# Kernel tuning notes

Measured on AMD Instinct MI355X. Metric: run time of the kernel, lower is better.

## Reference

```python
import jax, jax.numpy as jnp
import numpy as np

N = 100000   # nodes
D = 128      # embedding_dim
E = 1600000  # edges
L = 3        # num_layers


def setup_inputs() -> dict:
    key = jax.random.key(0)
    ks = jax.random.split(key, 10)
    s = 1.0 / np.sqrt(D)
    def w(k, shape):
        return jax.random.uniform(k, shape, jnp.float32, -s, s)
    return {
        "x": jax.random.normal(ks[0], (N, D), jnp.float32),
        "edge_index": jax.random.randint(ks[1], (2, E), 0, N, jnp.int32),
        "Wp": w(ks[2], (L - 1, D, D)),   # project Linear weight (per layer)
        "bp": w(ks[3], (L - 1, D)),      # project Linear bias
        "Wl": w(ks[4], (L - 1, D, D)),   # lin_l (aggregated neighbors)
        "bl": w(ks[5], (L - 1, D)),
        "Wr": w(ks[6], (L - 1, D, D)),   # lin_r (root, no bias)
        "Wl_out": w(ks[7], (D, D)),
        "bl_out": w(ks[8], (D,)),
        "Wr_out": w(ks[9], (D, D)),
    }


def _sage(x, src, dst, inv_deg, Wl, bl, Wr, Wp=None, bp=None, normalize=False):
    # PyG SAGEConv: project applies to messages only; root term uses original x.
    h = jax.nn.relu(x @ Wp.T + bp) if Wp is not None else x
    agg = jax.ops.segment_sum(h[src], dst, num_segments=N) * inv_deg  # mean aggr
    out = agg @ Wl.T + bl + x @ Wr.T
    if normalize:
        out = out / jnp.maximum(
            jnp.linalg.norm(out, axis=-1, keepdims=True), 1e-12)
    return out


def reference(x, edge_index, Wp, bp, Wl, bl, Wr, Wl_out, bl_out, Wr_out):
    src, dst = edge_index[0], edge_index[1]
    deg = jax.ops.segment_sum(jnp.ones((src.shape[0],), x.dtype), dst,
                              num_segments=N)
    inv_deg = (1.0 / jnp.maximum(deg, 1.0))[:, None]  # isolated nodes -> 0 agg
    for i in range(L - 1):
        x = jax.nn.relu(
            _sage(x, src, dst, inv_deg, Wl[i], bl[i], Wr[i], Wp[i], bp[i],
                  normalize=True))
    return _sage(x, src, dst, inv_deg, Wl_out, bl_out, Wr_out)
```

## Files before the change

kernel.cpp:

```cpp
#include <hip/hip_runtime.h>
#include <math.h>

#define D 128

typedef short s8v __attribute__((ext_vector_type(8)));
typedef float f32x4 __attribute__((ext_vector_type(4)));
typedef unsigned short u16x8 __attribute__((ext_vector_type(8)));

__device__ __forceinline__ unsigned short f2bf(float f) {
  union { float f; unsigned u; } c; c.f = f;
  unsigned u = c.u;
  unsigned r = (u + 0x7fffu + ((u >> 16) & 1u)) >> 16;
  return (unsigned short)r;
}

__device__ __forceinline__ void gload_lds16(const void* g, void* l) {
  __builtin_amdgcn_global_load_lds((const __attribute__((address_space(1))) void*)g,
                                   (__attribute__((address_space(3))) void*)l, 16, 0, 0);
}

__global__ __launch_bounds__(256) void k_prep(const float* __restrict__ Wp,
                                              const float* __restrict__ Wl,
                                              const float* __restrict__ Wr,
                                              const float* __restrict__ Wlo,
                                              const float* __restrict__ Wro,
                                              unsigned short* __restrict__ Wb,
                                              const int* __restrict__ dst,
                                              int* __restrict__ bucketCnt, int E_) {
  int t = threadIdx.x;
  if (blockIdx.x < 128) {
    int i = blockIdx.x * 256 + t;
    const float* s;
    int off;
    if (i < 8192)       { s = Wp;  off = 0; }
    else if (i < 16384) { s = Wl;  off = 8192; }
    else if (i < 24576) { s = Wr;  off = 16384; }
    else if (i < 28672) { s = Wlo; off = 24576; }
    else                { s = Wro; off = 28672; }
    float4 a = ((const float4*)s)[i - off];
    ushort4 o;
    o.x = f2bf(a.x); o.y = f2bf(a.y); o.z = f2bf(a.z); o.w = f2bf(a.w);
    ((ushort4*)Wb)[i] = o;
  } else {
    __shared__ int hist[512];
    hist[t] = 0; hist[t + 256] = 0;
    __syncthreads();
    int base = (blockIdx.x - 128) * 4096;
#pragma unroll
    for (int i = 0; i < 16; i++) {
      int e = base + i * 256 + t;
      if (e < E_) atomicAdd(&hist[dst[e] >> 8], 1);
    }
    __syncthreads();
    int c = hist[t];       if (c) atomicAdd(&bucketCnt[t], c);
    c = hist[t + 256];     if (c) atomicAdd(&bucketCnt[t + 256], c);
  }
}

__global__ __launch_bounds__(512) void k_bucket_scan(const int* __restrict__ cnt,
                                                     int* __restrict__ base,
                                                     int* __restrict__ cursor,
                                                     int* __restrict__ row_start,
                                                     int n, int E_) {
  __shared__ int bs[512];
  int t = threadIdx.x;
  int orig = cnt[t];
  bs[t] = orig;
  __syncthreads();
  for (int off = 1; off < 512; off <<= 1) {
    int x = (t >= off) ? bs[t - off] : 0;
    __syncthreads();
    bs[t] += x;
    __syncthreads();
  }
  int ex = bs[t] - orig;
  base[t] = ex;
  cursor[t] = ex;
  if (t == 511) base[512] = bs[511];
  if (t == 0) row_start[n] = E_;
}

__global__ __launch_bounds__(1024) void k_partA(const int* __restrict__ src,
                                                const int* __restrict__ dst,
                                                int* __restrict__ cursor,
                                                unsigned* __restrict__ pairs, int E_) {
  __shared__ int hist[512];
  __shared__ int gbase[512];
  int t = threadIdx.x;
  int base = blockIdx.x * 16384;
  if (t < 512) hist[t] = 0;
  __syncthreads();
  unsigned p_[16];
  int k_[16];
#pragma unroll
  for (int i = 0; i < 16; i++) {
    int e = base + i * 1024 + t;
    if (e < E_) {
      int s = src[e], d = dst[e];
      p_[i] = ((unsigned)s << 8) | (unsigned)(d & 255);
      k_[i] = d >> 8;
      atomicAdd(&hist[k_[i]], 1);
    } else {
      k_[i] = -1;
    }
  }
  __syncthreads();
  if (t < 512) {
    int c = hist[t];
    gbase[t] = c ? atomicAdd(&cursor[t], c) : 0;
    hist[t] = 0;
  }
  __syncthreads();
#pragma unroll
  for (int i = 0; i < 16; i++) {
    if (k_[i] >= 0) {
      int r = atomicAdd(&hist[k_[i]], 1);
      pairs[gbase[k_[i]] + r] = p_[i];
    }
  }
}

__device__ __forceinline__ int swz_chunk(int r, int c) { return (r << 4) + (c ^ (r & 7)); }

__global__ __launch_bounds__(1024, 4) void k_proj0B(const float* __restrict__ Av,
                                                    const unsigned short* __restrict__ W,
                                                    const float* __restrict__ bias,
                                                    unsigned short* __restrict__ out,
                                                    unsigned short* __restrict__ xb_out,
                                                    const unsigned* __restrict__ pairs,
                                                    const int* __restrict__ bucketBase,
                                                    int* __restrict__ row_start,
                                                    int* __restrict__ csr,
                                                    int n, int nP) {
  __shared__ __align__(16) unsigned short Wlds[128 * 128];
  __shared__ int cnt[256];
  __shared__ int scn[256];
  int t = threadIdx.x;

  if ((int)blockIdx.x < nP) {
    int wv = t >> 6, l = t & 63, lg = l >> 4, ln = l & 15;
    int rb = blockIdx.x * 256 + wv * 16;
    int arow = rb + ln;
    if (arow >= n) arow = n - 1;

    s8v a[4];
    const float* Af = Av + (size_t)arow * D + lg * 8;
#pragma unroll
    for (int ks = 0; ks < 4; ++ks) {
      float4 f0 = *(const float4*)(Af + ks * 32);
      float4 f1 = *(const float4*)(Af + ks * 32 + 4);
      s8v av;
      av[0] = (short)f2bf(f0.x); av[1] = (short)f2bf(f0.y);
      av[2] = (short)f2bf(f0.z); av[3] = (short)f2bf(f0.w);
      av[4] = (short)f2bf(f1.x); av[5] = (short)f2bf(f1.y);
      av[6] = (short)f2bf(f1.z); av[7] = (short)f2bf(f1.w);
      a[ks] = av;
      *(s8v*)(xb_out + (size_t)arow * D + lg * 8 + ks * 32) = av;
    }

#pragma unroll
    for (int i = 0; i < 2; ++i) {
      int idx = t + i * 1024;
      int r = idx >> 4, k = idx & 15;
      int c = k ^ (r & 7);
      gload_lds16(W + r * 128 + c * 8, &Wlds[idx * 8]);
    }
    __syncthreads();

    f32x4 acc[8];
#pragma unroll
    for (int f = 0; f < 8; ++f) acc[f] = (f32x4){0.f, 0.f, 0.f, 0.f};
#pragma unroll
    for (int ks = 0; ks < 4; ++ks) {
#pragma unroll
      for (int f = 0; f < 8; ++f) {
        s8v b = *(const s8v*)&Wlds[swz_chunk(f * 16 + ln, ks * 4 + lg) * 8];
        acc[f] = __builtin_amdgcn_mfma_f32_16x16x32_bf16(a[ks], b, acc[f], 0, 0, 0);
      }
    }

#pragma unroll
    for (int r = 0; r < 4; ++r) {
      int gr = rb + 4 * lg + r;
      if (gr < n) {
#pragma unroll
        for (int f = 0; f < 8; ++f) {
          int c = f * 16 + ln;
          float v = acc[f][r] + bias[c];
          v = fmaxf(v, 0.f);
          out[(size_t)gr * D + c] = f2bf(v);
        }
      }
    }
  } else {
    int k = blockIdx.x - nP;
    int node0 = k << 8;
    int pbeg = bucketBase[k], pend = bucketBase[k + 1];
    if (t < 256) cnt[t] = 0;
    __syncthreads();
    for (int p = pbeg + t; p < pend; p += 1024) atomicAdd(&cnt[pairs[p] & 255], 1);
    __syncthreads();
    int c = 0;
    if (t < 256) { c = cnt[t]; scn[t] = c; }
    __syncthreads();
    for (int off = 1; off < 256; off <<= 1) {
      int xv = 0;
      if (t < 256 && t >= off) xv = scn[t - off];
      __syncthreads();
      if (t < 256) scn[t] += xv;
      __syncthreads();
    }
    if (t < 256) {
      int ex = scn[t] - c;
      int node = node0 + t;
      if (node < n) row_start[node] = pbeg + ex;
      cnt[t] = pbeg + ex;
    }
    __syncthreads();
    for (int p = pbeg + t; p < pend; p += 1024) {
      unsigned pr = pairs[p];
      int slot = atomicAdd(&cnt[pr & 255], 1);
      csr[slot] = (int)(pr >> 8);
    }
  }
}

__global__ __launch_bounds__(256) void k_aggregate(const unsigned short* __restrict__ h,
                                                   unsigned short* __restrict__ agg,
                                                   const int* __restrict__ row_start,
                                                   const int* __restrict__ csr, int n) {
  int node = (blockIdx.x * 256 + threadIdx.x) >> 4;
  int li = threadIdx.x & 15;
  if (node >= n) return;
  int rs0 = row_start[node];
  int dc = row_start[node + 1] - rs0;
  const int* ce = csr + rs0;
  const char* base = (const char*)h + li * 16;

  float accL[4], accH[4];
#pragma unroll
  for (int q = 0; q < 4; q++) { accL[q] = 0.f; accH[q] = 0.f; }

#define ACCR(v)                                                        \
  {                                                                    \
    unsigned dw[4] = {(v).x, (v).y, (v).z, (v).w};                     \
    _Pragma("unroll") for (int q = 0; q < 4; q++) {                    \
      accL[q] += __uint_as_float(dw[q] << 16);                         \
      accH[q] += __uint_as_float(dw[q] & 0xffff0000u);                 \
    }                                                                  \
  }

  int e = 0;
  bool more = (3 < dc);
  int s0 = 0, s1 = 0, s2 = 0, s3 = 0;
  if (more) { s0 = ce[0]; s1 = ce[1]; s2 = ce[2]; s3 = ce[3]; }
  while (more) {
    uint4 v0 = *(const uint4*)(base + (size_t)s0 * 256);
    uint4 v1 = *(const uint4*)(base + (size_t)s1 * 256);
    uint4 v2 = *(const uint4*)(base + (size_t)s2 * 256);
    uint4 v3 = *(const uint4*)(base + (size_t)s3 * 256);
    e += 4;
    more = (e + 3 < dc);
    if (more) { s0 = ce[e]; s1 = ce[e + 1]; s2 = ce[e + 2]; s3 = ce[e + 3]; }
    ACCR(v0); ACCR(v1); ACCR(v2); ACCR(v3);
  }
  if (e < dc)     { uint4 v = *(const uint4*)(base + (size_t)ce[e] * 256);     ACCR(v); }
  if (e + 1 < dc) { uint4 v = *(const uint4*)(base + (size_t)ce[e + 1] * 256); ACCR(v); }
  if (e + 2 < dc) { uint4 v = *(const uint4*)(base + (size_t)ce[e + 2] * 256); ACCR(v); }
#undef ACCR

  float iv = 1.0f / (float)(dc > 0 ? dc : 1);
  u16x8 o;
#pragma unroll
  for (int q = 0; q < 4; q++) {
    o[2 * q] = f2bf(accL[q] * iv);
    o[2 * q + 1] = f2bf(accH[q] * iv);
  }
  *(u16x8*)(agg + (size_t)node * D + li * 8) = o;
}

__global__ __launch_bounds__(512, 4) void k_gemm_proj(const unsigned short* __restrict__ A,
                                                      const unsigned short* __restrict__ W,
                                                      const float* __restrict__ bias,
                                                      unsigned short* __restrict__ out,
                                                      int n) {
  __shared__ __align__(16) unsigned short Wlds[128 * 128];
  int t = threadIdx.x;
  int wv = t >> 6, l = t & 63, lg = l >> 4, ln = l & 15;
  int rb = blockIdx.x * 128 + wv * 16;
  int arow = rb + ln;
  if (arow >= n) arow = n - 1;

  const s8v* Ap = (const s8v*)(A + (size_t)arow * D + lg * 8);
  s8v a[4];
#pragma unroll
  for (int ks = 0; ks < 4; ++ks) a[ks] = Ap[ks * 4];

#pragma unroll
  for (int i = 0; i < 4; ++i) {
    int idx = t + i * 512;
    int r = idx >> 4, k = idx & 15;
    int c = k ^ (r & 7);
    gload_lds16(W + r * 128 + c * 8, &Wlds[idx * 8]);
  }
  __syncthreads();

  f32x4 acc[8];
#pragma unroll
  for (int f = 0; f < 8; ++f) acc[f] = (f32x4){0.f, 0.f, 0.f, 0.f};
#pragma unroll
  for (int ks = 0; ks < 4; ++ks) {
#pragma unroll
    for (int f = 0; f < 8; ++f) {
      s8v b = *(const s8v*)&Wlds[swz_chunk(f * 16 + ln, ks * 4 + lg) * 8];
      acc[f] = __builtin_amdgcn_mfma_f32_16x16x32_bf16(a[ks], b, acc[f], 0, 0, 0);
    }
  }

#pragma unroll
  for (int r = 0; r < 4; ++r) {
    int gr = rb + 4 * lg + r;
    if (gr < n) {
#pragma unroll
      for (int f = 0; f < 8; ++f) {
        int c = f * 16 + ln;
        float v = acc[f][r] + bias[c];
        v = fmaxf(v, 0.f);
        out[(size_t)gr * D + c] = f2bf(v);
      }
    }
  }
}

template <int MODE>
__global__ __launch_bounds__(512, 4) void k_gemm_dual(const unsigned short* __restrict__ A1,
                                                      const unsigned short* __restrict__ W1,
                                                      const float* __restrict__ bias,
                                                      const unsigned short* __restrict__ A2,
                                                      const unsigned short* __restrict__ W2,
                                                      void* __restrict__ outv, int n) {
  __shared__ __align__(16) unsigned short Wlds[2 * 128 * 128];
  int t = threadIdx.x;
  int wv = t >> 6, l = t & 63, lg = l >> 4, ln = l & 15;
  int rb = blockIdx.x * 128 + wv * 16;
  int arow = rb + ln;
  if (arow >= n) arow = n - 1;
  const s8v* A1p = (const s8v*)(A1 + (size_t)arow * D + lg * 8);
  const s8v* A2p = (const s8v*)(A2 + (size_t)arow * D + lg * 8);
  s8v a1[4], a2[4];
#pragma unroll
  for (int ks = 0; ks < 4; ++ks) { a1[ks] = A1p[ks * 4]; a2[ks] = A2p[ks * 4]; }

#pragma unroll
  for (int i = 0; i < 8; ++i) {
    int idx = t + i * 512;
    int mat = idx >> 11;
    int rem = idx & 2047;
    int r = rem >> 4, k = rem & 15;
    int c = k ^ (r & 7);
    const unsigned short* src = (mat ? W2 : W1) + r * 128 + c * 8;
    gload_lds16(src, &Wlds[idx * 8]);
  }
  __syncthreads();

  f32x4 acc[8];
#pragma unroll
  for (int f = 0; f < 8; ++f) acc[f] = (f32x4){0.f, 0.f, 0.f, 0.f};

#pragma unroll
  for (int ks = 0; ks < 4; ++ks) {
#pragma unroll
    for (int f = 0; f < 8; ++f) {
      int ch = swz_chunk(f * 16 + ln, ks * 4 + lg) * 8;
      s8v b1 = *(const s8v*)&Wlds[ch];
      s8v b2 = *(const s8v*)&Wlds[16384 + ch];
      acc[f] = __builtin_amdgcn_mfma_f32_16x16x32_bf16(a1[ks], b1, acc[f], 0, 0, 0);
      acc[f] = __builtin_amdgcn_mfma_f32_16x16x32_bf16(a2[ks], b2, acc[f], 0, 0, 0);
    }
  }

#pragma unroll
  for (int r = 0; r < 4; ++r) {
    int gr = rb + 4 * lg + r;
    float v[8];
#pragma unroll
    for (int f = 0; f < 8; ++f) v[f] = acc[f][r] + bias[f * 16 + ln];
    if (MODE == 0) {
      float ss = 0.f;
#pragma unroll
      for (int f = 0; f < 8; ++f) ss += v[f] * v[f];
      ss += __shfl_xor(ss, 1);
      ss += __shfl_xor(ss, 2);
      ss += __shfl_xor(ss, 4);
      ss += __shfl_xor(ss, 8);
      float sc = 1.0f / fmaxf(sqrtf(ss), 1e-12f);
      if (gr < n) {
        unsigned short* out = (unsigned short*)outv;
#pragma unroll
        for (int f = 0; f < 8; ++f) {
          float o = fmaxf(v[f] * sc, 0.f);
          out[(size_t)gr * D + f * 16 + ln] = f2bf(o);
        }
      }
    } else {
      if (gr < n) {
        float* out = (float*)outv;
#pragma unroll
        for (int f = 0; f < 8; ++f) out[(size_t)gr * D + f * 16 + ln] = v[f];
      }
    }
  }
}

extern "C" void kernel_launch(void* const* d_in, const int* in_sizes, int n_in,
                              void* d_out, int out_size, void* d_ws, size_t ws_size,
                              hipStream_t stream) {
  const float* x   = (const float*)d_in[0];
  const int*   ei  = (const int*)d_in[1];
  const float* Wp  = (const float*)d_in[2];
  const float* bp  = (const float*)d_in[3];
  const float* Wl  = (const float*)d_in[4];
  const float* bl  = (const float*)d_in[5];
  const float* Wr  = (const float*)d_in[6];
  const float* Wlo = (const float*)d_in[7];
  const float* blo = (const float*)d_in[8];
  const float* Wro = (const float*)d_in[9];

  const int N = in_sizes[0] / D;
  const int E = in_sizes[1] / 2;
  const int* srcIdx = ei;
  const int* dstIdx = ei + E;

  const size_t ND = (size_t)N * D;

  unsigned short* xb   = (unsigned short*)d_ws;
  unsigned short* h    = xb + ND;
  unsigned short* aggB = h + ND;
  unsigned short* x2   = aggB + ND;
  unsigned short* Wb   = x2 + ND;
  int* row_start  = (int*)(Wb + 8 * 16384);
  int* bucketCnt  = row_start + N + 1;
  int* bucketBase = bucketCnt + 512;
  int* cursor     = bucketBase + 513;
  int* csr        = cursor + 512;

  unsigned* pairs = (unsigned*)aggB;

  unsigned short* Wpb0 = Wb;
  unsigned short* Wpb1 = Wb + 16384;
  unsigned short* Wlb0 = Wb + 2 * 16384;
  unsigned short* Wlb1 = Wb + 3 * 16384;
  unsigned short* Wrb0 = Wb + 4 * 16384;
  unsigned short* Wrb1 = Wb + 5 * 16384;
  unsigned short* Wlob = Wb + 6 * 16384;
  unsigned short* Wrob = Wb + 7 * 16384;

  unsigned short* x1 = (unsigned short*)d_out;

  int gG  = (N + 127) / 128;
  int gP  = (N + 255) / 256;
  int gAg = (N * 16 + 255) / 256;
  int KB  = (N + 255) / 256;
  int gBC = (E + 4095) / 4096;
  int gA  = (E + 16383) / 16384;

  hipMemsetAsync(bucketCnt, 0, 512 * sizeof(int), stream);
  k_prep<<<128 + gBC, 256, 0, stream>>>(Wp, Wl, Wr, Wlo, Wro, Wb, dstIdx, bucketCnt, E);

  k_bucket_scan<<<1, 512, 0, stream>>>(bucketCnt, bucketBase, cursor, row_start, N, E);
  k_partA<<<gA, 1024, 0, stream>>>(srcIdx, dstIdx, cursor, pairs, E);

  k_proj0B<<<gP + KB, 1024, 0, stream>>>(x, Wpb0, bp, h, xb,
                                         pairs, bucketBase, row_start, csr, N, gP);

  k_aggregate<<<gAg, 256, 0, stream>>>(h, aggB, row_start, csr, N);
  k_gemm_dual<0><<<gG, 512, 0, stream>>>(aggB, Wlb0, bl, xb, Wrb0, (void*)x1, N);

  k_gemm_proj<<<gG, 512, 0, stream>>>(x1, Wpb1, bp + D, h, N);
  k_aggregate<<<gAg, 256, 0, stream>>>(h, aggB, row_start, csr, N);
  k_gemm_dual<0><<<gG, 512, 0, stream>>>(aggB, Wlb1, bl + D, x1, Wrb1, (void*)x2, N);

  k_aggregate<<<gAg, 256, 0, stream>>>(x2, aggB, row_start, csr, N);
  k_gemm_dual<1><<<gG, 512, 0, stream>>>(aggB, Wlob, blo, x2, Wrob, d_out, N);
}
```

Baseline: 323.6 us.

## Fuse neighbor aggregation with dual GEMM and regroup CSR build kernels

Aggregation is fused with the following lin_l/lin_r dual GEMM: each 256-thread block gathers 16 nodes' neighbor means into a swizzled LDS tile, then four waves each compute two 16-column output fragments, with L2 normalization reduced across waves through shared memory. This removes the bf16 agg buffer write and reread per layer and one launch per layer. Weights are now read straight from global memory per block instead of being staged in LDS, and each block does only a small GEMM, which adds redundant weight traffic. Separately, partition-A is co-scheduled with the layer-0 projection in one launch, and partition-B becomes its own kernel.

```diff
diff --git a/kernel.cpp b/kernel.cpp
--- a/kernel.cpp
+++ b/kernel.cpp
@@ -80,66 +80,60 @@
   if (t == 0) row_start[n] = E_;
 }
 
-__global__ __launch_bounds__(1024) void k_partA(const int* __restrict__ src,
-                                                const int* __restrict__ dst,
-                                                int* __restrict__ cursor,
-                                                unsigned* __restrict__ pairs, int E_) {
+__device__ __forceinline__ int swz_chunk(int r, int c) { return (r << 4) + (c ^ (r & 7)); }
+
+__global__ __launch_bounds__(1024, 2) void k_partA_proj(const int* __restrict__ src,
+                                                        const int* __restrict__ dst,
+                                                        int* __restrict__ cursor,
+                                                        unsigned* __restrict__ pairs,
+                                                        int E_,
+                                                        const float* __restrict__ Av,
+                                                        const unsigned short* __restrict__ W,
+                                                        const float* __restrict__ bias,
+                                                        unsigned short* __restrict__ out,
+                                                        unsigned short* __restrict__ xb_out,
+                                                        int n, int nA) {
   __shared__ int hist[512];
   __shared__ int gbase[512];
+  __shared__ __align__(16) unsigned short Wlds[128 * 128];
   int t = threadIdx.x;
-  int base = blockIdx.x * 16384;
-  if (t < 512) hist[t] = 0;
-  __syncthreads();
-  unsigned p_[16];
-  int k_[16];
-#pragma unroll
-  for (int i = 0; i < 16; i++) {
-    int e = base + i * 1024 + t;
-    if (e < E_) {
-      int s = src[e], d = dst[e];
-      p_[i] = ((unsigned)s << 8) | (unsigned)(d & 255);
-      k_[i] = d >> 8;
-      atomicAdd(&hist[k_[i]], 1);
-    } else {
-      k_[i] = -1;
-    }
-  }
-  __syncthreads();
-  if (t < 512) {
-    int c = hist[t];
-    gbase[t] = c ? atomicAdd(&cursor[t], c) : 0;
-    hist[t] = 0;
-  }
-  __syncthreads();
-#pragma unroll
-  for (int i = 0; i < 16; i++) {
-    if (k_[i] >= 0) {
-      int r = atomicAdd(&hist[k_[i]], 1);
-      pairs[gbase[k_[i]] + r] = p_[i];
-    }
-  }
-}
-
-__device__ __forceinline__ int swz_chunk(int r, int c) { return (r << 4) + (c ^ (r & 7)); }
-
-__global__ __launch_bounds__(1024, 4) void k_proj0B(const float* __restrict__ Av,
-                                                    const unsigned short* __restrict__ W,
-                                                    const float* __restrict__ bias,
-                                                    unsigned short* __restrict__ out,
-                                                    unsigned short* __restrict__ xb_out,
-                                                    const unsigned* __restrict__ pairs,
-                                                    const int* __restrict__ bucketBase,
-                                                    int* __restrict__ row_start,
-                                                    int* __restrict__ csr,
-                                                    int n, int nP) {
-  __shared__ __align__(16) unsigned short Wlds[128 * 128];
-  __shared__ int cnt[256];
-  __shared__ int scn[256];
-  int t = threadIdx.x;
-
-  if ((int)blockIdx.x < nP) {
+
+  if ((int)blockIdx.x < nA) {
+    int base = blockIdx.x * 16384;
+    if (t < 512) hist[t] = 0;
+    __syncthreads();
+    unsigned p_[16];
+    int k_[16];
+#pragma unroll
+    for (int i = 0; i < 16; i++) {
+      int e = base + i * 1024 + t;
+      if (e < E_) {
+        int s = src[e], d = dst[e];
+        p_[i] = ((unsigned)s << 8) | (unsigned)(d & 255);
+        k_[i] = d >> 8;
+        atomicAdd(&hist[k_[i]], 1);
+      } else {
+        k_[i] = -1;
+      }
+    }
+    __syncthreads();
+    if (t < 512) {
+      int c = hist[t];
+      gbase[t] = c ? atomicAdd(&cursor[t], c) : 0;
+      hist[t] = 0;
+    }
+    __syncthreads();
+#pragma unroll
+    for (int i = 0; i < 16; i++) {
+      if (k_[i] >= 0) {
+        int r = atomicAdd(&hist[k_[i]], 1);
+        pairs[gbase[k_[i]] + r] = p_[i];
+      }
+    }
+  } else {
+    int bid = blockIdx.x - nA;
     int wv = t >> 6, l = t & 63, lg = l >> 4, ln = l & 15;
-    int rb = blockIdx.x * 256 + wv * 16;
+    int rb = bid * 256 + wv * 16;
     int arow = rb + ln;
     if (arow >= n) arow = n - 1;
 
@@ -192,50 +186,68 @@
         }
       }
     }
-  } else {
-    int k = blockIdx.x - nP;
-    int node0 = k << 8;
-    int pbeg = bucketBase[k], pend = bucketBase[k + 1];
-    if (t < 256) cnt[t] = 0;
-    __syncthreads();
-    for (int p = pbeg + t; p < pend; p += 1024) atomicAdd(&cnt[pairs[p] & 255], 1);
-    __syncthreads();
-    int c = 0;
-    if (t < 256) { c = cnt[t]; scn[t] = c; }
-    __syncthreads();
-    for (int off = 1; off < 256; off <<= 1) {
-      int xv = 0;
-      if (t < 256 && t >= off) xv = scn[t - off];
-      __syncthreads();
-      if (t < 256) scn[t] += xv;
-      __syncthreads();
-    }
-    if (t < 256) {
-      int ex = scn[t] - c;
-      int node = node0 + t;
-      if (node < n) row_start[node] = pbeg + ex;
-      cnt[t] = pbeg + ex;
-    }
-    __syncthreads();
-    for (int p = pbeg + t; p < pend; p += 1024) {
-      unsigned pr = pairs[p];
-      int slot = atomicAdd(&cnt[pr & 255], 1);
-      csr[slot] = (int)(pr >> 8);
-    }
-  }
-}
-
-__global__ __launch_bounds__(256) void k_aggregate(const unsigned short* __restrict__ h,
-                                                   unsigned short* __restrict__ agg,
-                                                   const int* __restrict__ row_start,
-                                                   const int* __restrict__ csr, int n) {
-  int node = (blockIdx.x * 256 + threadIdx.x) >> 4;
-  int li = threadIdx.x & 15;
-  if (node >= n) return;
+  }
+}
+
+__global__ __launch_bounds__(1024) void k_partB(const unsigned* __restrict__ pairs,
+                                                const int* __restrict__ bucketBase,
+                                                int* __restrict__ row_start,
+                                                int* __restrict__ csr, int n) {
+  __shared__ int cnt[256];
+  __shared__ int scn[256];
+  int k = blockIdx.x, t = threadIdx.x;
+  int node0 = k << 8;
+  int pbeg = bucketBase[k], pend = bucketBase[k + 1];
+  if (t < 256) cnt[t] = 0;
+  __syncthreads();
+  for (int p = pbeg + t; p < pend; p += 1024) atomicAdd(&cnt[pairs[p] & 255], 1);
+  __syncthreads();
+  int c = 0;
+  if (t < 256) { c = cnt[t]; scn[t] = c; }
+  __syncthreads();
+  for (int off = 1; off < 256; off <<= 1) {
+    int xv = 0;
+    if (t < 256 && t >= off) xv = scn[t - off];
+    __syncthreads();
+    if (t < 256) scn[t] += xv;
+    __syncthreads();
+  }
+  if (t < 256) {
+    int ex = scn[t] - c;
+    int node = node0 + t;
+    if (node < n) row_start[node] = pbeg + ex;
+    cnt[t] = pbeg + ex;
+  }
+  __syncthreads();
+  for (int p = pbeg + t; p < pend; p += 1024) {
+    unsigned pr = pairs[p];
+    int slot = atomicAdd(&cnt[pr & 255], 1);
+    csr[slot] = (int)(pr >> 8);
+  }
+}
+
+template <int MODE>
+__global__ __launch_bounds__(256) void k_agg_dual(const unsigned short* __restrict__ h,
+                                                  const int* __restrict__ row_start,
+                                                  const int* __restrict__ csr,
+                                                  const unsigned short* __restrict__ W1,
+                                                  const float* __restrict__ bias,
+                                                  const unsigned short* __restrict__ A2,
+                                                  const unsigned short* __restrict__ W2,
+                                                  void* __restrict__ outv, int n) {
+  __shared__ __align__(16) unsigned short tile[16 * 128];
+  __shared__ float ssP[4][16];
+  int t = threadIdx.x;
+  int nodeLoc = t >> 4;
+  int li = t & 15;
+  int node0 = blockIdx.x * 16;
+  int node = node0 + nodeLoc;
+  if (node >= n) node = n - 1;
+
   int rs0 = row_start[node];
   int dc = row_start[node + 1] - rs0;
   const int* ce = csr + rs0;
-  const char* base = (const char*)h + li * 16;
+  const char* gbase = (const char*)h + li * 16;
 
   float accL[4], accH[4];
 #pragma unroll
@@ -255,28 +267,106 @@
   int s0 = 0, s1 = 0, s2 = 0, s3 = 0;
   if (more) { s0 = ce[0]; s1 = ce[1]; s2 = ce[2]; s3 = ce[3]; }
   while (more) {
-    uint4 v0 = *(const uint4*)(base + (size_t)s0 * 256);
-    uint4 v1 = *(const uint4*)(base + (size_t)s1 * 256);
-    uint4 v2 = *(const uint4*)(base + (size_t)s2 * 256);
-    uint4 v3 = *(const uint4*)(base + (size_t)s3 * 256);
+    uint4 v0 = *(const uint4*)(gbase + (size_t)s0 * 256);
+    uint4 v1 = *(const uint4*)(gbase + (size_t)s1 * 256);
+    uint4 v2 = *(const uint4*)(gbase + (size_t)s2 * 256);
+    uint4 v3 = *(const uint4*)(gbase + (size_t)s3 * 256);
     e += 4;
     more = (e + 3 < dc);
     if (more) { s0 = ce[e]; s1 = ce[e + 1]; s2 = ce[e + 2]; s3 = ce[e + 3]; }
     ACCR(v0); ACCR(v1); ACCR(v2); ACCR(v3);
   }
-  if (e < dc)     { uint4 v = *(const uint4*)(base + (size_t)ce[e] * 256);     ACCR(v); }
-  if (e + 1 < dc) { uint4 v = *(const uint4*)(base + (size_t)ce[e + 1] * 256); ACCR(v); }
-  if (e + 2 < dc) { uint4 v = *(const uint4*)(base + (size_t)ce[e + 2] * 256); ACCR(v); }
+  if (e < dc)     { uint4 v = *(const uint4*)(gbase + (size_t)ce[e] * 256);     ACCR(v); }
+  if (e + 1 < dc) { uint4 v = *(const uint4*)(gbase + (size_t)ce[e + 1] * 256); ACCR(v); }
+  if (e + 2 < dc) { uint4 v = *(const uint4*)(gbase + (size_t)ce[e + 2] * 256); ACCR(v); }
 #undef ACCR
 
   float iv = 1.0f / (float)(dc > 0 ? dc : 1);
-  u16x8 o;
-#pragma unroll
-  for (int q = 0; q < 4; q++) {
-    o[2 * q] = f2bf(accL[q] * iv);
-    o[2 * q + 1] = f2bf(accH[q] * iv);
-  }
-  *(u16x8*)(agg + (size_t)node * D + li * 8) = o;
+  {
+    u16x8 o;
+#pragma unroll
+    for (int q = 0; q < 4; q++) {
+      o[2 * q] = f2bf(accL[q] * iv);
+      o[2 * q + 1] = f2bf(accH[q] * iv);
+    }
+    *(u16x8*)&tile[swz_chunk(nodeLoc, li) * 8] = o;
+  }
+  __syncthreads();
+
+  int wv = t >> 6, l = t & 63, lg = l >> 4, ln = l & 15;
+  int a2row = node0 + ln;
+  if (a2row >= n) a2row = n - 1;
+  s8v a1[4], a2[4];
+#pragma unroll
+  for (int ks = 0; ks < 4; ++ks) {
+    a1[ks] = *(const s8v*)&tile[swz_chunk(ln, ks * 4 + lg) * 8];
+    a2[ks] = *(const s8v*)(A2 + (size_t)a2row * D + lg * 8 + ks * 32);
+  }
+
+  f32x4 acc[2];
+  acc[0] = (f32x4){0.f, 0.f, 0.f, 0.f};
+  acc[1] = (f32x4){0.f, 0.f, 0.f, 0.f};
+#pragma unroll
+  for (int ks = 0; ks < 4; ++ks) {
+#pragma unroll
+    for (int ff = 0; ff < 2; ++ff) {
+      int f = wv * 2 + ff;
+      s8v b1 = *(const s8v*)(W1 + (size_t)(f * 16 + ln) * D + lg * 8 + ks * 32);
+      s8v b2 = *(const s8v*)(W2 + (size_t)(f * 16 + ln) * D + lg * 8 + ks * 32);
+      acc[ff] = __builtin_amdgcn_mfma_f32_16x16x32_bf16(a1[ks], b1, acc[ff], 0, 0, 0);
+      acc[ff] = __builtin_amdgcn_mfma_f32_16x16x32_bf16(a2[ks], b2, acc[ff], 0, 0, 0);
+    }
+  }
+
+  float v[2][4];
+#pragma unroll
+  for (int ff = 0; ff < 2; ++ff)
+#pragma unroll
+    for (int r = 0; r < 4; ++r) v[ff][r] = acc[ff][r] + bias[(wv * 2 + ff) * 16 + ln];
+
+  if (MODE == 0) {
+    float ssr[4];
+#pragma unroll
+    for (int r = 0; r < 4; ++r) ssr[r] = v[0][r] * v[0][r] + v[1][r] * v[1][r];
+#pragma unroll
+    for (int r = 0; r < 4; ++r) {
+      ssr[r] += __shfl_xor(ssr[r], 1);
+      ssr[r] += __shfl_xor(ssr[r], 2);
+      ssr[r] += __shfl_xor(ssr[r], 4);
+      ssr[r] += __shfl_xor(ssr[r], 8);
+    }
+    if (ln == 0) {
+#pragma unroll
+      for (int r = 0; r < 4; ++r) ssP[wv][lg * 4 + r] = ssr[r];
+    }
+    __syncthreads();
+    unsigned short* out = (unsigned short*)outv;
+#pragma unroll
+    for (int r = 0; r < 4; ++r) {
+      int row = lg * 4 + r;
+      int gr = node0 + row;
+      float ss = ssP[0][row] + ssP[1][row] + ssP[2][row] + ssP[3][row];
+      float sc = 1.0f / fmaxf(sqrtf(ss), 1e-12f);
+      if (gr < n) {
+#pragma unroll
+        for (int ff = 0; ff < 2; ++ff) {
+          float o = fmaxf(v[ff][r] * sc, 0.f);
+          out[(size_t)gr * D + (wv * 2 + ff) * 16 + ln] = f2bf(o);
+        }
+      }
+    }
+  } else {
+    float* out = (float*)outv;
+#pragma unroll
+    for (int r = 0; r < 4; ++r) {
+      int gr = node0 + lg * 4 + r;
+      if (gr < n) {
+#pragma unroll
+        for (int ff = 0; ff < 2; ++ff)
+          out[(size_t)gr * D + (wv * 2 + ff) * 16 + ln] = v[ff][r];
+      }
+    }
+  }
 }
 
 __global__ __launch_bounds__(512, 4) void k_gemm_proj(const unsigned short* __restrict__ A,
@@ -327,86 +417,6 @@
         float v = acc[f][r] + bias[c];
         v = fmaxf(v, 0.f);
         out[(size_t)gr * D + c] = f2bf(v);
-      }
-    }
-  }
-}
-
-template <int MODE>
-__global__ __launch_bounds__(512, 4) void k_gemm_dual(const unsigned short* __restrict__ A1,
-                                                      const unsigned short* __restrict__ W1,
-                                                      const float* __restrict__ bias,
-                                                      const unsigned short* __restrict__ A2,
-                                                      const unsigned short* __restrict__ W2,
-                                                      void* __restrict__ outv, int n) {
-  __shared__ __align__(16) unsigned short Wlds[2 * 128 * 128];
-  int t = threadIdx.x;
-  int wv = t >> 6, l = t & 63, lg = l >> 4, ln = l & 15;
-  int rb = blockIdx.x * 128 + wv * 16;
-  int arow = rb + ln;
-  if (arow >= n) arow = n - 1;
-  const s8v* A1p = (const s8v*)(A1 + (size_t)arow * D + lg * 8);
-  const s8v* A2p = (const s8v*)(A2 + (size_t)arow * D + lg * 8);
-  s8v a1[4], a2[4];
-#pragma unroll
-  for (int ks = 0; ks < 4; ++ks) { a1[ks] = A1p[ks * 4]; a2[ks] = A2p[ks * 4]; }
-
-#pragma unroll
-  for (int i = 0; i < 8; ++i) {
-    int idx = t + i * 512;
-    int mat = idx >> 11;
-    int rem = idx & 2047;
-    int r = rem >> 4, k = rem & 15;
-    int c = k ^ (r & 7);
-    const unsigned short* src = (mat ? W2 : W1) + r * 128 + c * 8;
-    gload_lds16(src, &Wlds[idx * 8]);
-  }
-  __syncthreads();
-
-  f32x4 acc[8];
-#pragma unroll
-  for (int f = 0; f < 8; ++f) acc[f] = (f32x4){0.f, 0.f, 0.f, 0.f};
-
-#pragma unroll
-  for (int ks = 0; ks < 4; ++ks) {
-#pragma unroll
-    for (int f = 0; f < 8; ++f) {
-      int ch = swz_chunk(f * 16 + ln, ks * 4 + lg) * 8;
-      s8v b1 = *(const s8v*)&Wlds[ch];
-      s8v b2 = *(const s8v*)&Wlds[16384 + ch];
-      acc[f] = __builtin_amdgcn_mfma_f32_16x16x32_bf16(a1[ks], b1, acc[f], 0, 0, 0);
-      acc[f] = __builtin_amdgcn_mfma_f32_16x16x32_bf16(a2[ks], b2, acc[f], 0, 0, 0);
-    }
-  }
-
-#pragma unroll
-  for (int r = 0; r < 4; ++r) {
-    int gr = rb + 4 * lg + r;
-    float v[8];
-#pragma unroll
-    for (int f = 0; f < 8; ++f) v[f] = acc[f][r] + bias[f * 16 + ln];
-    if (MODE == 0) {
-      float ss = 0.f;
-#pragma unroll
-      for (int f = 0; f < 8; ++f) ss += v[f] * v[f];
-      ss += __shfl_xor(ss, 1);
-      ss += __shfl_xor(ss, 2);
-      ss += __shfl_xor(ss, 4);
-      ss += __shfl_xor(ss, 8);
-      float sc = 1.0f / fmaxf(sqrtf(ss), 1e-12f);
-      if (gr < n) {
-        unsigned short* out = (unsigned short*)outv;
-#pragma unroll
-        for (int f = 0; f < 8; ++f) {
-          float o = fmaxf(v[f] * sc, 0.f);
-          out[(size_t)gr * D + f * 16 + ln] = f2bf(o);
-        }
-      }
-    } else {
-      if (gr < n) {
-        float* out = (float*)outv;
-#pragma unroll
-        for (int f = 0; f < 8; ++f) out[(size_t)gr * D + f * 16 + ln] = v[f];
       }
     }
   }
@@ -459,27 +469,26 @@
 
   int gG  = (N + 127) / 128;
   int gP  = (N + 255) / 256;
-  int gAg = (N * 16 + 255) / 256;
+  int gF  = (N + 15) / 16;
   int KB  = (N + 255) / 256;
   int gBC = (E + 4095) / 4096;
   int gA  = (E + 16383) / 16384;
 
   hipMemsetAsync(bucketCnt, 0, 512 * sizeof(int), stream);
   k_prep<<<128 + gBC, 256, 0, stream>>>(Wp, Wl, Wr, Wlo, Wro, Wb, dstIdx, bucketCnt, E);
-
   k_bucket_scan<<<1, 512, 0, stream>>>(bucketCnt, bucketBase, cursor, row_start, N, E);
-  k_partA<<<gA, 1024, 0, stream>>>(srcIdx, dstIdx, cursor, pairs, E);
-
-  k_proj0B<<<gP + KB, 1024, 0, stream>>>(x, Wpb0, bp, h, xb,
-                                         pairs, bucketBase, row_start, csr, N, gP);
-
-  k_aggregate<<<gAg, 256, 0, stream>>>(h, aggB, row_start, csr, N);
-  k_gemm_dual<0><<<gG, 512, 0, stream>>>(aggB, Wlb0, bl, xb, Wrb0, (void*)x1, N);
+
+  k_partA_proj<<<gA + gP, 1024, 0, stream>>>(srcIdx, dstIdx, cursor, pairs, E,
+                                             x, Wpb0, bp, h, xb, N, gA);
+  k_partB<<<KB, 1024, 0, stream>>>(pairs, bucketBase, row_start, csr, N);
+
+  k_agg_dual<0><<<gF, 256, 0, stream>>>(h, row_start, csr, Wlb0, bl, xb, Wrb0,
+                                        (void*)x1, N);
 
   k_gemm_proj<<<gG, 512, 0, stream>>>(x1, Wpb1, bp + D, h, N);
-  k_aggregate<<<gAg, 256, 0, stream>>>(h, aggB, row_start, csr, N);
-  k_gemm_dual<0><<<gG, 512, 0, stream>>>(aggB, Wlb1, bl + D, x1, Wrb1, (void*)x2, N);
-
-  k_aggregate<<<gAg, 256, 0, stream>>>(x2, aggB, row_start, csr, N);
-  k_gemm_dual<1><<<gG, 512, 0, stream>>>(aggB, Wlob, blo, x2, Wrob, d_out, N);
-}
+  k_agg_dual<0><<<gF, 256, 0, stream>>>(h, row_start, csr, Wlb1, bl + D, x1, Wrb1,
+                                        (void*)x2, N);
+
+  k_agg_dual<1><<<gF, 256, 0, stream>>>(x2, row_start, csr, Wlob, blo, x2, Wrob,
+                                        d_out, N);
+}
```

New measurement: 379.3 us. 1.17x slower.

## Regroup setup kernels and fuse layer-1 combine with layer-2 projection

Applied to the files above, without the earlier changes.

The edge partition pass (partA) now runs in the same launch as the first-layer input projection, and the CSR finalize pass (partB) becomes its own kernel. The layer-1 dual GEMM with normalize/ReLU is fused with the layer-2 projection GEMM, so the block rereads its own freshly written x1 rows instead of launching a separate kernel. This removes one launch and a round trip of x1 between kernels, at the cost of more LDS per block and a second serial GEMM phase inside the fused kernel. The fused kernel relies on a vmcnt wait plus a barrier so each block sees its own global writes of x1.

```diff
diff --git a/kernel.cpp b/kernel.cpp
--- a/kernel.cpp
+++ b/kernel.cpp
@@ -80,66 +80,60 @@
   if (t == 0) row_start[n] = E_;
 }
 
-__global__ __launch_bounds__(1024) void k_partA(const int* __restrict__ src,
-                                                const int* __restrict__ dst,
-                                                int* __restrict__ cursor,
-                                                unsigned* __restrict__ pairs, int E_) {
+__device__ __forceinline__ int swz_chunk(int r, int c) { return (r << 4) + (c ^ (r & 7)); }
+
+__global__ __launch_bounds__(1024, 2) void k_partA_proj(const int* __restrict__ src,
+                                                        const int* __restrict__ dst,
+                                                        int* __restrict__ cursor,
+                                                        unsigned* __restrict__ pairs,
+                                                        int E_,
+                                                        const float* __restrict__ Av,
+                                                        const unsigned short* __restrict__ W,
+                                                        const float* __restrict__ bias,
+                                                        unsigned short* __restrict__ out,
+                                                        unsigned short* __restrict__ xb_out,
+                                                        int n, int nA) {
   __shared__ int hist[512];
   __shared__ int gbase[512];
+  __shared__ __align__(16) unsigned short Wlds[128 * 128];
   int t = threadIdx.x;
-  int base = blockIdx.x * 16384;
-  if (t < 512) hist[t] = 0;
-  __syncthreads();
-  unsigned p_[16];
-  int k_[16];
-#pragma unroll
-  for (int i = 0; i < 16; i++) {
-    int e = base + i * 1024 + t;
-    if (e < E_) {
-      int s = src[e], d = dst[e];
-      p_[i] = ((unsigned)s << 8) | (unsigned)(d & 255);
-      k_[i] = d >> 8;
-      atomicAdd(&hist[k_[i]], 1);
-    } else {
-      k_[i] = -1;
-    }
-  }
-  __syncthreads();
-  if (t < 512) {
-    int c = hist[t];
-    gbase[t] = c ? atomicAdd(&cursor[t], c) : 0;
-    hist[t] = 0;
-  }
-  __syncthreads();
-#pragma unroll
-  for (int i = 0; i < 16; i++) {
-    if (k_[i] >= 0) {
-      int r = atomicAdd(&hist[k_[i]], 1);
-      pairs[gbase[k_[i]] + r] = p_[i];
-    }
-  }
-}
-
-__device__ __forceinline__ int swz_chunk(int r, int c) { return (r << 4) + (c ^ (r & 7)); }
-
-__global__ __launch_bounds__(1024, 4) void k_proj0B(const float* __restrict__ Av,
-                                                    const unsigned short* __restrict__ W,
-                                                    const float* __restrict__ bias,
-                                                    unsigned short* __restrict__ out,
-                                                    unsigned short* __restrict__ xb_out,
-                                                    const unsigned* __restrict__ pairs,
-                                                    const int* __restrict__ bucketBase,
-                                                    int* __restrict__ row_start,
-                                                    int* __restrict__ csr,
-                                                    int n, int nP) {
-  __shared__ __align__(16) unsigned short Wlds[128 * 128];
-  __shared__ int cnt[256];
-  __shared__ int scn[256];
-  int t = threadIdx.x;
-
-  if ((int)blockIdx.x < nP) {
+
+  if ((int)blockIdx.x < nA) {
+    int base = blockIdx.x * 16384;
+    if (t < 512) hist[t] = 0;
+    __syncthreads();
+    unsigned p_[16];
+    int k_[16];
+#pragma unroll
+    for (int i = 0; i < 16; i++) {
+      int e = base + i * 1024 + t;
+      if (e < E_) {
+        int s = src[e], d = dst[e];
+        p_[i] = ((unsigned)s << 8) | (unsigned)(d & 255);
+        k_[i] = d >> 8;
+        atomicAdd(&hist[k_[i]], 1);
+      } else {
+        k_[i] = -1;
+      }
+    }
+    __syncthreads();
+    if (t < 512) {
+      int c = hist[t];
+      gbase[t] = c ? atomicAdd(&cursor[t], c) : 0;
+      hist[t] = 0;
+    }
+    __syncthreads();
+#pragma unroll
+    for (int i = 0; i < 16; i++) {
+      if (k_[i] >= 0) {
+        int r = atomicAdd(&hist[k_[i]], 1);
+        pairs[gbase[k_[i]] + r] = p_[i];
+      }
+    }
+  } else {
+    int bid = blockIdx.x - nA;
     int wv = t >> 6, l = t & 63, lg = l >> 4, ln = l & 15;
-    int rb = blockIdx.x * 256 + wv * 16;
+    int rb = bid * 256 + wv * 16;
     int arow = rb + ln;
     if (arow >= n) arow = n - 1;
 
@@ -192,36 +186,43 @@
         }
       }
     }
-  } else {
-    int k = blockIdx.x - nP;
-    int node0 = k << 8;
-    int pbeg = bucketBase[k], pend = bucketBase[k + 1];
-    if (t < 256) cnt[t] = 0;
-    __syncthreads();
-    for (int p = pbeg + t; p < pend; p += 1024) atomicAdd(&cnt[pairs[p] & 255], 1);
-    __syncthreads();
-    int c = 0;
-    if (t < 256) { c = cnt[t]; scn[t] = c; }
-    __syncthreads();
-    for (int off = 1; off < 256; off <<= 1) {
-      int xv = 0;
-      if (t < 256 && t >= off) xv = scn[t - off];
-      __syncthreads();
-      if (t < 256) scn[t] += xv;
-      __syncthreads();
-    }
-    if (t < 256) {
-      int ex = scn[t] - c;
-      int node = node0 + t;
-      if (node < n) row_start[node] = pbeg + ex;
-      cnt[t] = pbeg + ex;
-    }
-    __syncthreads();
-    for (int p = pbeg + t; p < pend; p += 1024) {
-      unsigned pr = pairs[p];
-      int slot = atomicAdd(&cnt[pr & 255], 1);
-      csr[slot] = (int)(pr >> 8);
-    }
+  }
+}
+
+__global__ __launch_bounds__(1024) void k_partB(const unsigned* __restrict__ pairs,
+                                                const int* __restrict__ bucketBase,
+                                                int* __restrict__ row_start,
+                                                int* __restrict__ csr, int n) {
+  __shared__ int cnt[256];
+  __shared__ int scn[256];
+  int k = blockIdx.x, t = threadIdx.x;
+  int node0 = k << 8;
+  int pbeg = bucketBase[k], pend = bucketBase[k + 1];
+  if (t < 256) cnt[t] = 0;
+  __syncthreads();
+  for (int p = pbeg + t; p < pend; p += 1024) atomicAdd(&cnt[pairs[p] & 255], 1);
+  __syncthreads();
+  int c = 0;
+  if (t < 256) { c = cnt[t]; scn[t] = c; }
+  __syncthreads();
+  for (int off = 1; off < 256; off <<= 1) {
+    int xv = 0;
+    if (t < 256 && t >= off) xv = scn[t - off];
+    __syncthreads();
+    if (t < 256) scn[t] += xv;
+    __syncthreads();
+  }
+  if (t < 256) {
+    int ex = scn[t] - c;
+    int node = node0 + t;
+    if (node < n) row_start[node] = pbeg + ex;
+    cnt[t] = pbeg + ex;
+  }
+  __syncthreads();
+  for (int p = pbeg + t; p < pend; p += 1024) {
+    unsigned pr = pairs[p];
+    int slot = atomicAdd(&cnt[pr & 255], 1);
+    csr[slot] = (int)(pr >> 8);
   }
 }
 
@@ -277,59 +278,6 @@
     o[2 * q + 1] = f2bf(accH[q] * iv);
   }
   *(u16x8*)(agg + (size_t)node * D + li * 8) = o;
-}
-
-__global__ __launch_bounds__(512, 4) void k_gemm_proj(const unsigned short* __restrict__ A,
-                                                      const unsigned short* __restrict__ W,
-                                                      const float* __restrict__ bias,
-                                                      unsigned short* __restrict__ out,
-                                                      int n) {
-  __shared__ __align__(16) unsigned short Wlds[128 * 128];
-  int t = threadIdx.x;
-  int wv = t >> 6, l = t & 63, lg = l >> 4, ln = l & 15;
-  int rb = blockIdx.x * 128 + wv * 16;
-  int arow = rb + ln;
-  if (arow >= n) arow = n - 1;
-
-  const s8v* Ap = (const s8v*)(A + (size_t)arow * D + lg * 8);
-  s8v a[4];
-#pragma unroll
-  for (int ks = 0; ks < 4; ++ks) a[ks] = Ap[ks * 4];
-
-#pragma unroll
-  for (int i = 0; i < 4; ++i) {
-    int idx = t + i * 512;
-    int r = idx >> 4, k = idx & 15;
-    int c = k ^ (r & 7);
-    gload_lds16(W + r * 128 + c * 8, &Wlds[idx * 8]);
-  }
-  __syncthreads();
-
-  f32x4 acc[8];
-#pragma unroll
-  for (int f = 0; f < 8; ++f) acc[f] = (f32x4){0.f, 0.f, 0.f, 0.f};
-#pragma unroll
-  for (int ks = 0; ks < 4; ++ks) {
-#pragma unroll
-    for (int f = 0; f < 8; ++f) {
-      s8v b = *(const s8v*)&Wlds[swz_chunk(f * 16 + ln, ks * 4 + lg) * 8];
-      acc[f] = __builtin_amdgcn_mfma_f32_16x16x32_bf16(a[ks], b, acc[f], 0, 0, 0);
-    }
-  }
-
-#pragma unroll
-  for (int r = 0; r < 4; ++r) {
-    int gr = rb + 4 * lg + r;
-    if (gr < n) {
-#pragma unroll
-      for (int f = 0; f < 8; ++f) {
-        int c = f * 16 + ln;
-        float v = acc[f][r] + bias[c];
-        v = fmaxf(v, 0.f);
-        out[(size_t)gr * D + c] = f2bf(v);
-      }
-    }
-  }
 }
 
 template <int MODE>
@@ -412,6 +360,123 @@
   }
 }
 
+__global__ __launch_bounds__(512, 4) void k_dual_proj(const unsigned short* __restrict__ A1,
+                                                      const unsigned short* __restrict__ W1,
+                                                      const float* __restrict__ bias,
+                                                      const unsigned short* __restrict__ A2,
+                                                      const unsigned short* __restrict__ W2,
+                                                      unsigned short* __restrict__ x1out,
+                                                      const unsigned short* __restrict__ Wp,
+                                                      const float* __restrict__ biasP,
+                                                      unsigned short* __restrict__ hout,
+                                                      int n) {
+  __shared__ __align__(16) unsigned short Wlds[2 * 128 * 128];
+  int t = threadIdx.x;
+  int wv = t >> 6, l = t & 63, lg = l >> 4, ln = l & 15;
+  int rb = blockIdx.x * 128 + wv * 16;
+  int arow = rb + ln;
+  if (arow >= n) arow = n - 1;
+  const s8v* A1p = (const s8v*)(A1 + (size_t)arow * D + lg * 8);
+  const s8v* A2p = (const s8v*)(A2 + (size_t)arow * D + lg * 8);
+  s8v a1[4], a2[4];
+#pragma unroll
+  for (int ks = 0; ks < 4; ++ks) { a1[ks] = A1p[ks * 4]; a2[ks] = A2p[ks * 4]; }
+
+#pragma unroll
+  for (int i = 0; i < 8; ++i) {
+    int idx = t + i * 512;
+    int mat = idx >> 11;
+    int rem = idx & 2047;
+    int r = rem >> 4, k = rem & 15;
+    int c = k ^ (r & 7);
+    const unsigned short* src = (mat ? W2 : W1) + r * 128 + c * 8;
+    gload_lds16(src, &Wlds[idx * 8]);
+  }
+  __syncthreads();
+
+  f32x4 acc[8];
+#pragma unroll
+  for (int f = 0; f < 8; ++f) acc[f] = (f32x4){0.f, 0.f, 0.f, 0.f};
+#pragma unroll
+  for (int ks = 0; ks < 4; ++ks) {
+#pragma unroll
+    for (int f = 0; f < 8; ++f) {
+      int ch = swz_chunk(f * 16 + ln, ks * 4 + lg) * 8;
+      s8v b1 = *(const s8v*)&Wlds[ch];
+      s8v b2 = *(const s8v*)&Wlds[16384 + ch];
+      acc[f] = __builtin_amdgcn_mfma_f32_16x16x32_bf16(a1[ks], b1, acc[f], 0, 0, 0);
+      acc[f] = __builtin_amdgcn_mfma_f32_16x16x32_bf16(a2[ks], b2, acc[f], 0, 0, 0);
+    }
+  }
+  __syncthreads();
+
+#pragma unroll
+  for (int i = 0; i < 4; ++i) {
+    int idx = t + i * 512;
+    int r = idx >> 4, k = idx & 15;
+    int c = k ^ (r & 7);
+    gload_lds16(Wp + r * 128 + c * 8, &Wlds[idx * 8]);
+  }
+
+#pragma unroll
+  for (int r = 0; r < 4; ++r) {
+    int gr = rb + 4 * lg + r;
+    float v[8];
+#pragma unroll
+    for (int f = 0; f < 8; ++f) v[f] = acc[f][r] + bias[f * 16 + ln];
+    float ss = 0.f;
+#pragma unroll
+    for (int f = 0; f < 8; ++f) ss += v[f] * v[f];
+    ss += __shfl_xor(ss, 1);
+    ss += __shfl_xor(ss, 2);
+    ss += __shfl_xor(ss, 4);
+    ss += __shfl_xor(ss, 8);
+    float sc = 1.0f / fmaxf(sqrtf(ss), 1e-12f);
+    if (gr < n) {
+#pragma unroll
+      for (int f = 0; f < 8; ++f) {
+        float o = fmaxf(v[f] * sc, 0.f);
+        x1out[(size_t)gr * D + f * 16 + ln] = f2bf(o);
+      }
+    }
+  }
+
+  asm volatile("s_waitcnt vmcnt(0)" ::: "memory");
+  __builtin_amdgcn_sched_barrier(0);
+  __syncthreads();
+
+  const s8v* Xp = (const s8v*)(x1out + (size_t)arow * D + lg * 8);
+  s8v ap[4];
+#pragma unroll
+  for (int ks = 0; ks < 4; ++ks) ap[ks] = Xp[ks * 4];
+
+  f32x4 acc2[8];
+#pragma unroll
+  for (int f = 0; f < 8; ++f) acc2[f] = (f32x4){0.f, 0.f, 0.f, 0.f};
+#pragma unroll
+  for (int ks = 0; ks < 4; ++ks) {
+#pragma unroll
+    for (int f = 0; f < 8; ++f) {
+      s8v b = *(const s8v*)&Wlds[swz_chunk(f * 16 + ln, ks * 4 + lg) * 8];
+      acc2[f] = __builtin_amdgcn_mfma_f32_16x16x32_bf16(ap[ks], b, acc2[f], 0, 0, 0);
+    }
+  }
+
+#pragma unroll
+  for (int r = 0; r < 4; ++r) {
+    int gr = rb + 4 * lg + r;
+    if (gr < n) {
+#pragma unroll
+      for (int f = 0; f < 8; ++f) {
+        int c = f * 16 + ln;
+        float v = acc2[f][r] + biasP[c];
+        v = fmaxf(v, 0.f);
+        hout[(size_t)gr * D + c] = f2bf(v);
+      }
+    }
+  }
+}
+
 extern "C" void kernel_launch(void* const* d_in, const int* in_sizes, int n_in,
                               void* d_out, int out_size, void* d_ws, size_t ws_size,
                               hipStream_t stream) {
@@ -466,17 +531,16 @@
 
   hipMemsetAsync(bucketCnt, 0, 512 * sizeof(int), stream);
   k_prep<<<128 + gBC, 256, 0, stream>>>(Wp, Wl, Wr, Wlo, Wro, Wb, dstIdx, bucketCnt, E);
-
   k_bucket_scan<<<1, 512, 0, stream>>>(bucketCnt, bucketBase, cursor, row_start, N, E);
-  k_partA<<<gA, 1024, 0, stream>>>(srcIdx, dstIdx, cursor, pairs, E);
-
-  k_proj0B<<<gP + KB, 1024, 0, stream>>>(x, Wpb0, bp, h, xb,
-                                         pairs, bucketBase, row_start, csr, N, gP);
+
+  k_partA_proj<<<gA + gP, 1024, 0, stream>>>(srcIdx, dstIdx, cursor, pairs, E,
+                                             x, Wpb0, bp, h, xb, N, gA);
+  k_partB<<<KB, 1024, 0, stream>>>(pairs, bucketBase, row_start, csr, N);
 
   k_aggregate<<<gAg, 256, 0, stream>>>(h, aggB, row_start, csr, N);
-  k_gemm_dual<0><<<gG, 512, 0, stream>>>(aggB, Wlb0, bl, xb, Wrb0, (void*)x1, N);
-
-  k_gemm_proj<<<gG, 512, 0, stream>>>(x1, Wpb1, bp + D, h, N);
+  k_dual_proj<<<gG, 512, 0, stream>>>(aggB, Wlb0, bl, xb, Wrb0, x1,
+                                      Wpb1, bp + D, h, N);
+
   k_aggregate<<<gAg, 256, 0, stream>>>(h, aggB, row_start, csr, N);
   k_gemm_dual<0><<<gG, 512, 0, stream>>>(aggB, Wlb1, bl + D, x1, Wrb1, (void*)x2, N);
 
```

Result: faster. 314.1 us (-2.9%).
